# Performance work log

Measured on AMD Instinct MI355X. Metric: run time of the kernel, lower is better.

## Reference

```python
import jax, jax.numpy as jnp
import numpy as np

N = 100_000   # nodes
E = 6_400_000 # edges
R = 90        # relations
NB = 3        # num_blocks


def setup_inputs() -> dict:
    key = jax.random.key(0)
    ks = jax.random.split(key, 10)
    x = jax.random.normal(ks[0], (N, 3), jnp.float32)
    edge_index = jax.random.randint(ks[1], (2, E), 0, N, dtype=jnp.int32)
    edge_type = jax.random.randint(ks[2], (E,), 0, R, dtype=jnp.int32)
    batch = jnp.zeros((N,), jnp.int32)  # single graph, as in source
    p = lambda k, shape: (jax.random.normal(k, shape, jnp.float32) * 0.1)
    # block-diagonal weights: [R, NB, in_b, out_b]
    W1, root1, b1 = p(ks[3], (R, NB, 1, 2)), p(ks[4], (3, 6)), jnp.zeros((6,), jnp.float32)
    W2, root2, b2 = p(ks[5], (R, NB, 2, 1)), p(ks[6], (6, 3)), jnp.zeros((3,), jnp.float32)
    W3, root3, b3 = p(ks[7], (R, NB, 1, 2)), p(ks[8], (3, 6)), jnp.zeros((6,), jnp.float32)
    return dict(x=x, edge_index=edge_index, batch=batch, edge_type=edge_type,
                W1=W1, root1=root1, b1=b1, W2=W2, root2=root2, b2=b2,
                W3=W3, root3=root3, b3=b3)


def _rgcn(x, src, dst, edge_type, W, root, bias, aggr):
    # block-diagonal per-relation transform of gathered source features
    nb, in_b, out_b = W.shape[1], W.shape[2], W.shape[3]
    xb = x[src].reshape(-1, nb, in_b)                      # [E, NB, in_b]
    msg = jnp.einsum('ebi,ebio->ebo', xb, W[edge_type])    # [E, NB, out_b]
    msg = msg.reshape(-1, nb * out_b)                      # [E, out]
    if aggr == 'mean':
        # per-(dst node, relation) normalization, as in FastRGCNConv
        comb = dst * R + edge_type                         # [E]
        cnt = jax.ops.segment_sum(jnp.ones((msg.shape[0],), msg.dtype), comb,
                                  num_segments=N * R)      # [N*R]
        msg = msg / jnp.clip(cnt[comb], 1.0)[:, None]
    agg = jax.ops.segment_sum(msg, dst, num_segments=N)    # [N, out]
    return agg + x @ root + bias


def reference(x, edge_index, batch, edge_type, W1, root1, b1, W2, root2, b2, W3, root3, b3):
    src, dst = edge_index[0], edge_index[1]
    h = jax.nn.relu(_rgcn(x, src, dst, edge_type, W1, root1, b1, 'mean'))
    # dropout is identity in eval mode
    h = jax.nn.relu(_rgcn(h, src, dst, edge_type, W2, root2, b2, 'add'))
    h = jax.nn.relu(_rgcn(h, src, dst, edge_type, W3, root3, b3, 'mean'))
    # global mean pool over batch (single graph here, kept general)
    num_graphs = 1
    s = jax.ops.segment_sum(h, batch, num_segments=num_graphs)
    c = jax.ops.segment_sum(jnp.ones((h.shape[0],), h.dtype), batch, num_segments=num_graphs)
    pooled = s / jnp.clip(c, 1.0)[:, None]
    return jax.nn.log_softmax(pooled, axis=1)
```

## Files before the change

kernel.cpp:

```cpp
#include <hip/hip_runtime.h>


#define NREL   90
#define BSH    7
#define BNODES 128
#define NBINS  1024
#define GCH    6912
#define STAGE  9216
#define MAXK   18
#define LPD    16

__device__ __forceinline__ float frelu(float v) { return v > 0.0f ? v : 0.0f; }

__launch_bounds__(512)
__global__ void padhist_k(const float* __restrict__ x, float4* __restrict__ x4, int N,
                          int gNp, const int* __restrict__ dst, int* __restrict__ bhist,
                          int* __restrict__ chist, int E) {
    int tid = threadIdx.x;
    if (blockIdx.x < gNp) {
        int i = blockIdx.x * 512 + tid;
        if (i < N) x4[i] = make_float4(x[3 * i], x[3 * i + 1], x[3 * i + 2], 0.0f);
        return;
    }
    __shared__ int h[NBINS];
    for (int i = tid; i < NBINS; i += 512) h[i] = 0;
    __syncthreads();
    int chunk = blockIdx.x - gNp;
    int e0 = chunk * GCH;
    int e1 = min(e0 + GCH, E);
    int e = e0 + tid;
    for (; e + 1536 < e1; e += 2048) {
        int d0 = dst[e], d1 = dst[e + 512], d2 = dst[e + 1024], d3 = dst[e + 1536];
        atomicAdd(&h[d0 >> BSH], 1); atomicAdd(&h[d1 >> BSH], 1);
        atomicAdd(&h[d2 >> BSH], 1); atomicAdd(&h[d3 >> BSH], 1);
    }
    for (; e < e1; e += 512) atomicAdd(&h[dst[e] >> BSH], 1);
    __syncthreads();
    int base = chunk * NBINS;
    for (int i = tid; i < NBINS; i += 512) {
        int c = h[i];
        chist[base + i] = c;
        if (c) atomicAdd(&bhist[i], c);
    }
}

__global__ void colscan_k(const int* __restrict__ bhist, int* __restrict__ bbase,
                          const int* __restrict__ chist, int* __restrict__ gbase,
                          int nchunks) {
    int b = blockIdx.x;
    int lane = threadIdx.x;
    int part = 0;
    int b0 = lane * 16;
#pragma unroll
    for (int k = 0; k < 16; k++) {
        int bin = b0 + k;
        int v = bhist[bin];
        if (bin < b) part += v;
    }
#pragma unroll
    for (int off = 32; off > 0; off >>= 1) part += __shfl_down(part, off);
    int run = __shfl(part, 0);
    if (lane == 0) bbase[b] = run;
    for (int c0 = 0; c0 < nchunks; c0 += 64) {
        int c = c0 + lane;
        int v = (c < nchunks) ? chist[(size_t)c * NBINS + b] : 0;
        int inc = v;
#pragma unroll
        for (int off = 1; off < 64; off <<= 1) {
            int u = __shfl_up(inc, off);
            if (lane >= off) inc += u;
        }
        if (c < nchunks) gbase[(size_t)c * NBINS + b] = run + inc - v;
        run += __shfl(inc, 63);
    }
}

__launch_bounds__(512)
__global__ void group_k(const int* __restrict__ src, const int* __restrict__ dst,
                        const int* __restrict__ et, const int* __restrict__ chist,
                        const int* __restrict__ gbase, unsigned* __restrict__ edges, int E) {
    __shared__ int s_cur[NBINS];
    __shared__ int s_gb2[NBINS];
    __shared__ unsigned s_pack[GCH];
    __shared__ unsigned short s_bkt[GCH];
    int tid = threadIdx.x;
    int chunk = blockIdx.x;
    int e0 = chunk * GCH;
    int cnt = min(GCH, E - e0);
    const int* crow = &chist[(size_t)chunk * NBINS];
    const int* grow = &gbase[(size_t)chunk * NBINS];
    if (tid < 64) {
        int loc[16];
        int s = 0;
        int b0 = tid * 16;
#pragma unroll
        for (int k = 0; k < 16; k++) { loc[k] = crow[b0 + k]; s += loc[k]; }
        int inc = s;
#pragma unroll
        for (int off = 1; off < 64; off <<= 1) {
            int u = __shfl_up(inc, off);
            if (tid >= off) inc += u;
        }
        int run = inc - s;
#pragma unroll
        for (int k = 0; k < 16; k++) { s_cur[b0 + k] = run; run += loc[k]; }
    }
    __syncthreads();
    for (int i = tid; i < NBINS; i += 512) s_gb2[i] = grow[i] - s_cur[i];
    __syncthreads();
    int q = tid;
    for (; q + 1536 < cnt; q += 2048) {
#pragma unroll
        for (int k = 0; k < 4; k++) {
            int e = e0 + q + k * 512;
            int d = dst[e];
            int b = d >> BSH;
            int p = atomicAdd(&s_cur[b], 1);
            if (p < GCH) {
                s_pack[p] = (unsigned)src[e] | ((unsigned)et[e] << 17) |
                            ((unsigned)(d & (BNODES - 1)) << 24);
                s_bkt[p] = (unsigned short)b;
            }
        }
    }
    for (; q < cnt; q += 512) {
        int e = e0 + q;
        int d = dst[e];
        int b = d >> BSH;
        int p = atomicAdd(&s_cur[b], 1);
        if (p < GCH) {
            s_pack[p] = (unsigned)src[e] | ((unsigned)et[e] << 17) |
                        ((unsigned)(d & (BNODES - 1)) << 24);
            s_bkt[p] = (unsigned short)b;
        }
    }
    __syncthreads();
    q = tid;
    for (; q + 1536 < cnt; q += 2048) {
#pragma unroll
        for (int k = 0; k < 4; k++) {
            int i = q + k * 512;
            edges[s_gb2[s_bkt[i]] + i] = s_pack[i];
        }
    }
    for (; q < cnt; q += 512) edges[s_gb2[s_bkt[q]] + q] = s_pack[q];
}

__launch_bounds__(512)
__global__ void sortb_l1_k(const int* __restrict__ bbase, const unsigned* __restrict__ edges,
                           unsigned* __restrict__ edges2, int* __restrict__ rowptr,
                           const float4* __restrict__ x4, const float* __restrict__ W,
                           const float* __restrict__ root, const float* __restrict__ bias,
                           float4* __restrict__ h1p, int N, int E) {
    __shared__ unsigned stage32[STAGE];
    __shared__ unsigned hist8w[BNODES * 90 / 4];
    __shared__ int hh[BNODES], cur[BNODES], base_[BNODES];
    __shared__ float4 w4[NREL * 2];
    int tid = threadIdx.x, b = blockIdx.x;
    for (int i = tid; i < BNODES * 90 / 4; i += 512) hist8w[i] = 0u;
    for (int i = tid; i < NREL * 2; i += 512) {
        int r = i >> 1;
        w4[i] = (i & 1) ? make_float4(W[r * 6 + 4], W[r * 6 + 5], 0.f, 0.f)
                        : make_float4(W[r * 6], W[r * 6 + 1], W[r * 6 + 2], W[r * 6 + 3]);
    }
    __syncthreads();
    int e0 = bbase[b];
    int e1 = (b + 1 < NBINS) ? bbase[b + 1] : E;
    int cnt = e1 - e0;
    unsigned rec[MAXK];
#pragma unroll
    for (int k = 0; k < MAXK; k++) {
        int idx = tid + k * 512;
        if (idx < cnt) {
            unsigned p = edges[e0 + idx];
            rec[k] = p;
            unsigned bi = (p >> 24) * 90u + ((p >> 17) & 127u);
            atomicAdd(&hist8w[bi >> 2], 1u << ((bi & 3) << 3));
        }
    }
    __syncthreads();
    if (tid < BNODES) {
        const unsigned char* h8 = (const unsigned char*)hist8w;
        unsigned s = 0;
        for (int k = 0; k < 90; k++) s += h8[tid * 90 + k];
        hh[tid] = (int)s;
    }
    __syncthreads();
    if (tid < 64) {
        int c0 = hh[2 * tid], c1 = hh[2 * tid + 1];
        int s = c0 + c1;
        int inc = s;
#pragma unroll
        for (int off = 1; off < 64; off <<= 1) {
            int u = __shfl_up(inc, off);
            if (tid >= off) inc += u;
        }
        int run = inc - s;
        base_[2 * tid] = run;          cur[2 * tid] = run;
        base_[2 * tid + 1] = run + c0; cur[2 * tid + 1] = run + c0;
    }
    __syncthreads();
    if (tid < BNODES) {
        int d = (b << BSH) + tid;
        if (d <= N) rowptr[d] = e0 + base_[tid];
    }
#pragma unroll
    for (int k = 0; k < MAXK; k++) {
        int idx = tid + k * 512;
        if (idx < cnt) {
            int pos = atomicAdd(&cur[rec[k] >> 24], 1);
            if (pos < STAGE) stage32[pos] = rec[k];
        }
    }
    __syncthreads();
    int grp = tid >> 4, l16 = tid & 15;
#pragma unroll
    for (int rd = 0; rd < 4; rd++) {
        int dL = grp + rd * 32;
        int segb = base_[dL];
        int sege = segb + hh[dL];
        if (sege > cnt) sege = cnt;
        float a0 = 0, a1 = 0, a2 = 0, a3 = 0, a4 = 0, a5 = 0;
        for (int q = segb + l16; q < sege; q += 16) {
            unsigned p = stage32[q];
            unsigned rel = (p >> 17) & 127u;
            unsigned bi = dL * 90u + rel;
            unsigned c = (hist8w[bi >> 2] >> ((bi & 3) << 3)) & 0xFFu;
            edges2[e0 + q] = (p & 0x00FFFFFFu) | (c << 24);
            float r = __builtin_amdgcn_rcpf((float)c);
            float4 xv = x4[p & 0x1FFFFu];
            unsigned rel2 = rel * 2u;
            float4 wa = w4[rel2], wb = w4[rel2 + 1];
            float x0 = xv.x * r, x1 = xv.y * r, x2 = xv.z * r;
            a0 += x0 * wa.x; a1 += x0 * wa.y;
            a2 += x1 * wa.z; a3 += x1 * wa.w;
            a4 += x2 * wb.x; a5 += x2 * wb.y;
        }
#pragma unroll
        for (int off = 8; off > 0; off >>= 1) {
            a0 += __shfl_down(a0, off); a1 += __shfl_down(a1, off); a2 += __shfl_down(a2, off);
            a3 += __shfl_down(a3, off); a4 += __shfl_down(a4, off); a5 += __shfl_down(a5, off);
        }
        if (l16 == 0) {
            int d = (b << BSH) + dL;
            if (d < N) {
                float4 xv = x4[d];
                float o[6] = {a0, a1, a2, a3, a4, a5};
#pragma unroll
                for (int j = 0; j < 6; j++)
                    o[j] = frelu(o[j] + xv.x * root[j] + xv.y * root[6 + j] +
                                 xv.z * root[12 + j] + bias[j]);
                h1p[d * 2]     = make_float4(o[0], o[1], o[2], o[3]);
                h1p[d * 2 + 1] = make_float4(o[4], o[5], 0.0f, 0.0f);
            }
        }
    }
}

__launch_bounds__(256)
__global__ void l2_g(const int* __restrict__ rowptr, const unsigned* __restrict__ sorted,
                     const float4* __restrict__ h1p, const float* __restrict__ W,
                     const float* __restrict__ root, const float* __restrict__ bias,
                     float4* __restrict__ h2p, int N) {
    __shared__ float4 w4[NREL * 2];
    for (int i = threadIdx.x; i < NREL * 2; i += 256) {
        int r = i >> 1;
        w4[i] = (i & 1) ? make_float4(W[r * 6 + 4], W[r * 6 + 5], 0.f, 0.f)
                        : make_float4(W[r * 6], W[r * 6 + 1], W[r * 6 + 2], W[r * 6 + 3]);
    }
    __syncthreads();
    int grp = threadIdx.x >> 4, l16 = threadIdx.x & 15;
    int d = blockIdx.x * LPD + grp;
    if (d >= N) return;
    int beg = rowptr[d], end = rowptr[d + 1];
    float a0 = 0, a1 = 0, a2 = 0;
    int i = beg + l16;
    for (; i + 48 < end; i += 64) {
        unsigned p[4];
        float4 ha[4], hb[4];
#pragma unroll
        for (int k = 0; k < 4; k++) p[k] = sorted[i + k * 16];
#pragma unroll
        for (int k = 0; k < 4; k++) {
            unsigned s = p[k] & 0x1FFFFu;
            ha[k] = h1p[2 * s]; hb[k] = h1p[2 * s + 1];
        }
#pragma unroll
        for (int k = 0; k < 4; k++) {
            unsigned rel2 = ((p[k] >> 17) & 127u) * 2u;
            float4 wa = w4[rel2], wb = w4[rel2 + 1];
            a0 += ha[k].x * wa.x + ha[k].y * wa.y;
            a1 += ha[k].z * wa.z + ha[k].w * wa.w;
            a2 += hb[k].x * wb.x + hb[k].y * wb.y;
        }
    }
    for (; i < end; i += 16) {
        unsigned p = sorted[i];
        unsigned s = p & 0x1FFFFu;
        float4 ha = h1p[2 * s], hb = h1p[2 * s + 1];
        unsigned rel2 = ((p >> 17) & 127u) * 2u;
        float4 wa = w4[rel2], wb = w4[rel2 + 1];
        a0 += ha.x * wa.x + ha.y * wa.y;
        a1 += ha.z * wa.z + ha.w * wa.w;
        a2 += hb.x * wb.x + hb.y * wb.y;
    }
#pragma unroll
    for (int off = 8; off > 0; off >>= 1) {
        a0 += __shfl_down(a0, off); a1 += __shfl_down(a1, off); a2 += __shfl_down(a2, off);
    }
    if (l16 == 0) {
        float4 ha = h1p[2 * d], hb = h1p[2 * d + 1];
        float hv[6] = {ha.x, ha.y, ha.z, ha.w, hb.x, hb.y};
        float o[3] = {a0, a1, a2};
#pragma unroll
        for (int j = 0; j < 3; j++) {
            float v = o[j] + bias[j];
#pragma unroll
            for (int k = 0; k < 6; k++) v += hv[k] * root[k * 3 + j];
            o[j] = frelu(v);
        }
        h2p[d] = make_float4(o[0], o[1], o[2], 0.0f);
    }
}

__launch_bounds__(256)
__global__ void l3_g(const int* __restrict__ rowptr, const unsigned* __restrict__ sorted,
                     const float4* __restrict__ h2p, const float* __restrict__ W,
                     const float* __restrict__ root, const float* __restrict__ bias,
                     const int* __restrict__ batch, float* __restrict__ partials, int N) {
    __shared__ float4 w4[NREL * 2];
    __shared__ float redsm[LPD][8];
    for (int i = threadIdx.x; i < NREL * 2; i += 256) {
        int r = i >> 1;
        w4[i] = (i & 1) ? make_float4(W[r * 6 + 4], W[r * 6 + 5], 0.f, 0.f)
                        : make_float4(W[r * 6], W[r * 6 + 1], W[r * 6 + 2], W[r * 6 + 3]);
    }
    __syncthreads();
    int grp = threadIdx.x >> 4, l16 = threadIdx.x & 15;
    int d = blockIdx.x * LPD + grp;
    float a0 = 0, a1 = 0, a2 = 0, a3 = 0, a4 = 0, a5 = 0;
    if (d < N) {
        int beg = rowptr[d], end = rowptr[d + 1];
        int i = beg + l16;
        for (; i + 48 < end; i += 64) {
            unsigned p[4];
            float4 xv[4];
#pragma unroll
            for (int k = 0; k < 4; k++) p[k] = sorted[i + k * 16];
#pragma unroll
            for (int k = 0; k < 4; k++) xv[k] = h2p[p[k] & 0x1FFFFu];
#pragma unroll
            for (int k = 0; k < 4; k++) {
                float r = __builtin_amdgcn_rcpf((float)(p[k] >> 24));
                unsigned rel2 = ((p[k] >> 17) & 127u) * 2u;
                float4 wa = w4[rel2], wb = w4[rel2 + 1];
                float x0 = xv[k].x * r, x1 = xv[k].y * r, x2 = xv[k].z * r;
                a0 += x0 * wa.x; a1 += x0 * wa.y;
                a2 += x1 * wa.z; a3 += x1 * wa.w;
                a4 += x2 * wb.x; a5 += x2 * wb.y;
            }
        }
        for (; i < end; i += 16) {
            unsigned p = sorted[i];
            float r = __builtin_amdgcn_rcpf((float)(p >> 24));
            float4 xv = h2p[p & 0x1FFFFu];
            unsigned rel2 = ((p >> 17) & 127u) * 2u;
            float4 wa = w4[rel2], wb = w4[rel2 + 1];
            float x0 = xv.x * r, x1 = xv.y * r, x2 = xv.z * r;
            a0 += x0 * wa.x; a1 += x0 * wa.y;
            a2 += x1 * wa.z; a3 += x1 * wa.w;
            a4 += x2 * wb.x; a5 += x2 * wb.y;
        }
    }
#pragma unroll
    for (int off = 8; off > 0; off >>= 1) {
        a0 += __shfl_down(a0, off); a1 += __shfl_down(a1, off); a2 += __shfl_down(a2, off);
        a3 += __shfl_down(a3, off); a4 += __shfl_down(a4, off); a5 += __shfl_down(a5, off);
    }
    if (l16 == 0) {
        float v[7] = {0, 0, 0, 0, 0, 0, 0};
        if (d < N && batch[d] == 0) {
            float4 xv = h2p[d];
            float o[6] = {a0, a1, a2, a3, a4, a5};
#pragma unroll
            for (int j = 0; j < 6; j++)
                v[j] = frelu(o[j] + xv.x * root[j] + xv.y * root[6 + j] +
                             xv.z * root[12 + j] + bias[j]);
            v[6] = 1.0f;
        }
#pragma unroll
        for (int k = 0; k < 7; k++) redsm[grp][k] = v[k];
    }
    __syncthreads();
    if (threadIdx.x < 7) {
        float t = 0;
#pragma unroll
        for (int g = 0; g < LPD; g++) t += redsm[g][threadIdx.x];
        partials[(size_t)blockIdx.x * 8 + threadIdx.x] = t;
    }
}

__global__ void pool_finalize(const float* __restrict__ partials, int nb,
                              float* __restrict__ out) {
    float v[7] = {0, 0, 0, 0, 0, 0, 0};
    for (int b = threadIdx.x; b < nb; b += blockDim.x) {
#pragma unroll
        for (int k = 0; k < 7; k++) v[k] += partials[(size_t)b * 8 + k];
    }
#pragma unroll
    for (int off = 32; off > 0; off >>= 1) {
#pragma unroll
        for (int k = 0; k < 7; k++) v[k] += __shfl_down(v[k], off);
    }
    __shared__ float sm[16][8];
    int wv = threadIdx.x >> 6, lane = threadIdx.x & 63;
    if (lane == 0) {
#pragma unroll
        for (int k = 0; k < 7; k++) sm[wv][k] = v[k];
    }
    __syncthreads();
    if (threadIdx.x == 0) {
        float t[7] = {0, 0, 0, 0, 0, 0, 0};
        int nw = blockDim.x >> 6;
        for (int q = 0; q < nw; q++) {
#pragma unroll
            for (int k = 0; k < 7; k++) t[k] += sm[q][k];
        }
        float c = t[6] < 1.0f ? 1.0f : t[6];
        float p[6], m = -1e30f;
#pragma unroll
        for (int j = 0; j < 6; j++) { p[j] = t[j] / c; m = fmaxf(m, p[j]); }
        float s = 0.0f;
#pragma unroll
        for (int j = 0; j < 6; j++) s += expf(p[j] - m);
        float lse = m + logf(s);
#pragma unroll
        for (int j = 0; j < 6; j++) out[j] = p[j] - lse;
    }
}

extern "C" void kernel_launch(void* const* d_in, const int* in_sizes, int n_in,
                              void* d_out, int out_size, void* d_ws, size_t ws_size,
                              hipStream_t stream) {
    const float* x     = (const float*)d_in[0];
    const int*   ei    = (const int*)d_in[1];
    const int*   batch = (const int*)d_in[2];
    const int*   etype = (const int*)d_in[3];
    const float* W1    = (const float*)d_in[4];
    const float* root1 = (const float*)d_in[5];
    const float* b1    = (const float*)d_in[6];
    const float* W2    = (const float*)d_in[7];
    const float* root2 = (const float*)d_in[8];
    const float* b2    = (const float*)d_in[9];
    const float* W3    = (const float*)d_in[10];
    const float* root3 = (const float*)d_in[11];
    const float* b3    = (const float*)d_in[12];

    const int N = in_sizes[0] / 3;
    const int E = in_sizes[1] / 2;
    const int* src = ei;
    const int* dst = ei + E;
    const int gG = (E + GCH - 1) / GCH;

    char* ws = (char*)d_ws;
    size_t off = 0;
    auto alloc = [&](size_t bytes) -> void* {
        void* p = ws + off;
        off += (bytes + 255) & ~(size_t)255;
        return p;
    };
    int*      bhist   = (int*)     alloc(NBINS * sizeof(int));
    size_t zero_bytes = off;
    int*      bbase   = (int*)     alloc((NBINS + 1) * sizeof(int));
    int*      chist   = (int*)     alloc((size_t)gG * NBINS * sizeof(int));
    int*      gbase   = (int*)     alloc((size_t)gG * NBINS * sizeof(int));
    unsigned* edges   = (unsigned*)alloc((size_t)E * sizeof(unsigned));
    unsigned* edges2  = (unsigned*)alloc((size_t)E * sizeof(unsigned));
    int*      rowptr  = (int*)     alloc((size_t)(N + 1) * sizeof(int));
    float4*   x4      = (float4*)  alloc((size_t)N * sizeof(float4));
    float4*   h1p     = (float4*)  alloc((size_t)N * 2 * sizeof(float4));
    float4*   h2p     = (float4*)  alloc((size_t)N * sizeof(float4));
    const int NBUCK = (N + BNODES - 1) >> BSH;
    const int gL    = (N + LPD - 1) / LPD;
    float*    partials = (float*)  alloc((size_t)gL * 8 * sizeof(float));

    hipMemsetAsync(d_ws, 0, zero_bytes, stream);

    const int gNp = (N + 511) / 512;

    padhist_k<<<gNp + gG, 512, 0, stream>>>(x, x4, N, gNp, dst, bhist, chist, E);
    colscan_k<<<NBINS, 64, 0, stream>>>(bhist, bbase, chist, gbase, gG);
    group_k<<<gG, 512, 0, stream>>>(src, dst, etype, chist, gbase, edges, E);
    sortb_l1_k<<<NBUCK, 512, 0, stream>>>(bbase, edges, edges2, rowptr,
                                          x4, W1, root1, b1, h1p, N, E);

    l2_g<<<gL, 256, 0, stream>>>(rowptr, edges2, h1p, W2, root2, b2, h2p, N);
    l3_g<<<gL, 256, 0, stream>>>(rowptr, edges2, h2p, W3, root3, b3, batch, partials, N);
    pool_finalize<<<1, 1024, 0, stream>>>(partials, gL, (float*)d_out);
}
```

Baseline: 340.7 us.

## Tile column scan over 16 bins per block and split per-node histogram sums

The column-scan kernel now gives each 256-thread block 16 bins instead of one bin per 64-thread wave. It loads chist rows into a shared tile so global reads and writes cover 16 contiguous ints, and it computes the bin prefix with a block-wide two-level scan. The per-node count reduction in the sort kernel is split across 4 threads per node with shared atomics instead of 128 threads each looping 90 bytes. The aim is to cut the scattered single-int column accesses and the serial reduction loop. The cost is a serial 16-thread scan over each 64-row tile, plus fewer blocks and therefore less parallelism.

After: 353.3 us. 1.04x slower.

```diff
diff --git a/kernel.cpp b/kernel.cpp
--- a/kernel.cpp
+++ b/kernel.cpp
@@ -44,34 +44,68 @@
     }
 }
 
+__launch_bounds__(256)
 __global__ void colscan_k(const int* __restrict__ bhist, int* __restrict__ bbase,
                           const int* __restrict__ chist, int* __restrict__ gbase,
                           int nchunks) {
-    int b = blockIdx.x;
-    int lane = threadIdx.x;
-    int part = 0;
-    int b0 = lane * 16;
-#pragma unroll
-    for (int k = 0; k < 16; k++) {
-        int bin = b0 + k;
-        int v = bhist[bin];
-        if (bin < b) part += v;
-    }
-#pragma unroll
-    for (int off = 32; off > 0; off >>= 1) part += __shfl_down(part, off);
-    int run = __shfl(part, 0);
-    if (lane == 0) bbase[b] = run;
-    for (int c0 = 0; c0 < nchunks; c0 += 64) {
-        int c = c0 + lane;
-        int v = (c < nchunks) ? chist[(size_t)c * NBINS + b] : 0;
-        int inc = v;
+    __shared__ int tile[64][16];
+    __shared__ int part4[256];
+    __shared__ int run[16];
+    int tid = threadIdx.x;
+    int b0 = blockIdx.x * 16;
+    int s4 = 0;
+    int p0 = tid * 4;
+#pragma unroll
+    for (int k = 0; k < 4; k++) s4 += bhist[p0 + k];
+    part4[tid] = s4;
+    __syncthreads();
+    if (tid < 64) {
+        int v0 = part4[tid * 4], v1 = part4[tid * 4 + 1];
+        int v2 = part4[tid * 4 + 2], v3 = part4[tid * 4 + 3];
+        int s = v0 + v1 + v2 + v3;
+        int inc = s;
 #pragma unroll
         for (int off = 1; off < 64; off <<= 1) {
             int u = __shfl_up(inc, off);
-            if (lane >= off) inc += u;
-        }
-        if (c < nchunks) gbase[(size_t)c * NBINS + b] = run + inc - v;
-        run += __shfl(inc, 63);
+            if (tid >= off) inc += u;
+        }
+        int r = inc - s;
+        part4[tid * 4] = r;
+        part4[tid * 4 + 1] = r + v0;
+        part4[tid * 4 + 2] = r + v0 + v1;
+        part4[tid * 4 + 3] = r + v0 + v1 + v2;
+    }
+    __syncthreads();
+    if (tid < 16) {
+        int b = b0 + tid;
+        int r = part4[b >> 2];
+        for (int k = (b & ~3); k < b; k++) r += bhist[k];
+        run[tid] = r;
+        bbase[b] = r;
+    }
+    __syncthreads();
+    for (int c0 = 0; c0 < nchunks; c0 += 64) {
+        int rows = min(64, nchunks - c0);
+        for (int k = tid; k < rows * 16; k += 256) {
+            int r = k >> 4, j = k & 15;
+            tile[r][j] = chist[(size_t)(c0 + r) * NBINS + b0 + j];
+        }
+        __syncthreads();
+        if (tid < 16) {
+            int acc = run[tid];
+            for (int r = 0; r < rows; r++) {
+                int v = tile[r][tid];
+                tile[r][tid] = acc;
+                acc += v;
+            }
+            run[tid] = acc;
+        }
+        __syncthreads();
+        for (int k = tid; k < rows * 16; k += 256) {
+            int r = k >> 4, j = k & 15;
+            gbase[(size_t)(c0 + r) * NBINS + b0 + j] = tile[r][j];
+        }
+        __syncthreads();
     }
 }
 
@@ -158,6 +192,7 @@
     __shared__ float4 w4[NREL * 2];
     int tid = threadIdx.x, b = blockIdx.x;
     for (int i = tid; i < BNODES * 90 / 4; i += 512) hist8w[i] = 0u;
+    if (tid < BNODES) hh[tid] = 0;
     for (int i = tid; i < NREL * 2; i += 512) {
         int r = i >> 1;
         w4[i] = (i & 1) ? make_float4(W[r * 6 + 4], W[r * 6 + 5], 0.f, 0.f)
@@ -179,11 +214,14 @@
         }
     }
     __syncthreads();
-    if (tid < BNODES) {
+    {
+        int dL = tid >> 2, part = tid & 3;
         const unsigned char* h8 = (const unsigned char*)hist8w;
+        int start = part * 23;
+        int len = (part == 3) ? 21 : 23;
         unsigned s = 0;
-        for (int k = 0; k < 90; k++) s += h8[tid * 90 + k];
-        hh[tid] = (int)s;
+        for (int k = 0; k < len; k++) s += h8[dL * 90 + start + k];
+        if (s) atomicAdd(&hh[dL], (int)s);
     }
     __syncthreads();
     if (tid < 64) {
@@ -489,7 +527,7 @@
     const int gNp = (N + 511) / 512;
 
     padhist_k<<<gNp + gG, 512, 0, stream>>>(x, x4, N, gNp, dst, bhist, chist, E);
-    colscan_k<<<NBINS, 64, 0, stream>>>(bhist, bbase, chist, gbase, gG);
+    colscan_k<<<NBINS / 16, 256, 0, stream>>>(bhist, bbase, chist, gbase, gG);
     group_k<<<gG, 512, 0, stream>>>(src, dst, etype, chist, gbase, edges, E);
     sortb_l1_k<<<NBUCK, 512, 0, stream>>>(bbase, edges, edges2, rowptr,
                                           x4, W1, root1, b1, h1p, N, E);
```
